# Performance work log

Measured on AMD Instinct MI355X. Metric: run time of the kernel, lower is better.

Reference implementation:

```python
import jax, jax.numpy as jnp
import numpy as np

N_V = 100000
N_E = 20000
NNZ = 1600000
D = 128


def setup_inputs() -> dict:
    key = jax.random.key(0)
    k1, k2, k3, k4, k5 = jax.random.split(key, 5)
    X = jax.random.normal(k1, (N_V, D), dtype=jnp.float32)
    W = jax.random.normal(k2, (D, D), dtype=jnp.float32) * (1.0 / np.sqrt(D))
    b = jax.random.normal(k3, (D,), dtype=jnp.float32) * 0.01
    v2e_src = jax.random.randint(k4, (NNZ,), 0, N_V, dtype=jnp.int32)
    v2e_dst = jax.random.randint(k5, (NNZ,), 0, N_E, dtype=jnp.int32)
    return {"X": X, "W": W, "b": b, "v2e_src": v2e_src, "v2e_dst": v2e_dst, "num_e": N_E}


def reference(X, W, b, v2e_src, v2e_dst, num_e):
    num_v = X.shape[0]
    ones = jnp.ones(v2e_src.shape[0], dtype=X.dtype)
    # node degrees (values of D_v diagonal) and hyperedge incidence counts
    deg_v = jax.ops.segment_sum(ones, v2e_src, num_segments=num_v)
    cnt_e = jax.ops.segment_sum(ones, v2e_dst, num_segments=num_e)

    # theta: linear layer
    Xt = X @ W.T + b  # [N_V, D]

    # v2e mean aggregation: per hyperedge, mean of incident vertex features
    Ysum = jax.ops.segment_sum(Xt[v2e_src], v2e_dst, num_segments=num_e)  # [N_E, D]
    Y = Ysum / jnp.maximum(cnt_e, 1.0)[:, None]

    # edge norm: torch scatter_reduce(reduce='mean', include_self=True) -> sum/(count+1)
    De_sum = jax.ops.segment_sum(deg_v[v2e_src], v2e_dst, num_segments=num_e)
    De = De_sum / (cnt_e + 1.0)
    De = jnp.where(De > 0, jax.lax.rsqrt(jnp.maximum(De, 1e-30)), 1.0)  # inf -> 1
    Y = De[:, None] * Y

    # e2v sum aggregation
    Xo = jax.ops.segment_sum(Y[v2e_dst], v2e_src, num_segments=num_v)  # [N_V, D]

    # D_v^{-1/2} sparse diagonal mm (zero-degree nodes -> 0)
    dvn = jnp.where(deg_v > 0, jax.lax.rsqrt(jnp.maximum(deg_v, 1e-30)), 0.0)
    Xo = dvn[:, None] * Xo

    # is_last=False: ReLU then dropout (dropout is identity in eval)
    return jax.nn.relu(Xo)
```

## Files before the change

### kernel.cpp

```cpp
#include <hip/hip_runtime.h>
#include <hip/hip_bf16.h>

#define NV 100000
#define NE 20000
#define DD 128
#define ESHIFT 7
#define VSHIFT 9
#define NBE 157
#define NBV 196
#define NBK 256
#define CHUNK 4096
#define CAPE 11264
#define CAPV 9216

using bf16 = __hip_bfloat16;

typedef __attribute__((ext_vector_type(8))) short frag_ab;
typedef __attribute__((ext_vector_type(4))) float frag_cd;

__device__ __forceinline__ float uas(unsigned u) { union { unsigned u; float f; } c; c.u = u; return c.f; }
__device__ __forceinline__ unsigned pk2(float lo, float hi) {
    bf16 l = __float2bfloat16(lo), h = __float2bfloat16(hi);
    return (unsigned)(*(unsigned short*)&l) | ((unsigned)(*(unsigned short*)&h) << 16);
}
__device__ __forceinline__ void accum8(float* a, uint4 x) {
    a[0] += uas(x.x << 16); a[1] += uas(x.x & 0xffff0000u);
    a[2] += uas(x.y << 16); a[3] += uas(x.y & 0xffff0000u);
    a[4] += uas(x.z << 16); a[5] += uas(x.z & 0xffff0000u);
    a[6] += uas(x.w << 16); a[7] += uas(x.w & 0xffff0000u);
}
__device__ __forceinline__ int wave_incl_scan(int v, int lane) {
#pragma unroll
    for (int o = 1; o < 64; o <<= 1) {
        int x = __shfl_up(v, o);
        if (lane >= o) v += x;
    }
    return v;
}

__global__ void init_cur(int* __restrict__ bcur_e, int* __restrict__ bcur_v) {
    int t = threadIdx.x;
    bcur_e[t] = t * CAPE;
    bcur_v[t] = t * CAPV;
}

__global__ __launch_bounds__(256) void partition_and_cvt(const int* __restrict__ src, const int* __restrict__ dst,
                                                         int* __restrict__ bcur_e, int* __restrict__ bcur_v,
                                                         unsigned* __restrict__ pairs_e, unsigned* __restrict__ pairs_v,
                                                         int nnz,
                                                         const float4* __restrict__ Xf, ushort4* __restrict__ Xb,
                                                         const float4* __restrict__ Wf, ushort4* __restrict__ Wb) {
    int nchunk = (nnz + CHUNK - 1) / CHUNK;
    int t = threadIdx.x;
    if ((int)blockIdx.x >= nchunk) {
        const int n4x = NV * DD / 4;
        const int n4w = DD * DD / 4;
        int i = ((int)blockIdx.x - nchunk) * 256 + t;
        if (i < n4x + n4w) {
            float4 v;
            ushort4 o;
            if (i < n4x) v = Xf[i]; else v = Wf[i - n4x];
            bf16 a = __float2bfloat16(v.x); o.x = *(unsigned short*)&a;
            bf16 b = __float2bfloat16(v.y); o.y = *(unsigned short*)&b;
            bf16 c = __float2bfloat16(v.z); o.z = *(unsigned short*)&c;
            bf16 d = __float2bfloat16(v.w); o.w = *(unsigned short*)&d;
            if (i < n4x) Xb[i] = o; else Wb[i - n4x] = o;
        }
        return;
    }
    __shared__ int cntA[NBK], cntB[NBK], pre1[NBK], loff[NBK], gbase[NBK], wsum[4];
    __shared__ int totValid;
    __shared__ unsigned stage[CHUNK];
    int sub = t >> 7;
    int lane = t & 63, wv = t >> 6;
    int base = blockIdx.x * CHUNK;
    unsigned p[16];
    int rk[16];
#pragma unroll
    for (int k = 0; k < 16; ++k) {
        int i = base + k * 256 + t;
        p[k] = (i < nnz) ? (((unsigned)src[i] << 15) | (unsigned)dst[i]) : 0xFFFFFFFFu;
    }

    cntA[t] = 0; cntB[t] = 0;
    __syncthreads();
#pragma unroll
    for (int k = 0; k < 16; ++k)
        if (p[k] != 0xFFFFFFFFu) {
            int b = (p[k] >> ESHIFT) & 0xFF;
            rk[k] = atomicAdd(sub ? &cntB[b] : &cntA[b], 1);
        }
    __syncthreads();
    {
        int a = cntA[t], bb = cntB[t];
        int tv = a + bb;
        pre1[t] = a;
        int incl = wave_incl_scan(tv, lane);
        if (lane == 63) wsum[wv] = incl;
        __syncthreads();
        if (t == 0) { int r = 0; for (int i = 0; i < 4; ++i) { int x = wsum[i]; wsum[i] = r; r += x; } }
        __syncthreads();
        int ex = incl - tv + wsum[wv];
        loff[t] = ex;
        gbase[t] = (tv > 0) ? atomicAdd(&bcur_e[t], tv) : 0;
        if (t == 255) totValid = ex + tv;
    }
    __syncthreads();
#pragma unroll
    for (int k = 0; k < 16; ++k)
        if (p[k] != 0xFFFFFFFFu) {
            int b = (p[k] >> ESHIFT) & 0xFF;
            stage[loff[b] + rk[k] + (sub ? pre1[b] : 0)] = p[k];
        }
    __syncthreads();
    for (int i = t; i < totValid; i += 256) {
        unsigned pp = stage[i];
        int b = (pp >> ESHIFT) & 0xFF;
        pairs_e[gbase[b] + i - loff[b]] = pp;
    }
    __syncthreads();

    cntA[t] = 0; cntB[t] = 0;
    __syncthreads();
#pragma unroll
    for (int k = 0; k < 16; ++k)
        if (p[k] != 0xFFFFFFFFu) {
            int b = p[k] >> 24;
            rk[k] = atomicAdd(sub ? &cntB[b] : &cntA[b], 1);
        }
    __syncthreads();
    {
        int a = cntA[t], bb = cntB[t];
        int tv = a + bb;
        pre1[t] = a;
        int incl = wave_incl_scan(tv, lane);
        if (lane == 63) wsum[wv] = incl;
        __syncthreads();
        if (t == 0) { int r = 0; for (int i = 0; i < 4; ++i) { int x = wsum[i]; wsum[i] = r; r += x; } }
        __syncthreads();
        int ex = incl - tv + wsum[wv];
        loff[t] = ex;
        gbase[t] = (tv > 0) ? atomicAdd(&bcur_v[t], tv) : 0;
        if (t == 255) totValid = ex + tv;
    }
    __syncthreads();
#pragma unroll
    for (int k = 0; k < 16; ++k)
        if (p[k] != 0xFFFFFFFFu) {
            int b = p[k] >> 24;
            stage[loff[b] + rk[k] + (sub ? pre1[b] : 0)] = p[k];
        }
    __syncthreads();
    for (int i = t; i < totValid; i += 256) {
        unsigned pp = stage[i];
        int b = pp >> 24;
        pairs_v[gbase[b] + i - loff[b]] = pp;
    }
}

__global__ __launch_bounds__(1024) void build_csr(const unsigned* __restrict__ pairs_e, const int* __restrict__ bcur_e,
                                                  int* __restrict__ off_e, int* __restrict__ end_e, int* __restrict__ e_src,
                                                  const unsigned* __restrict__ pairs_v, const int* __restrict__ bcur_v,
                                                  int* __restrict__ off_v, int* __restrict__ end_v, int* __restrict__ v_edge,
                                                  int* __restrict__ deg_v) {
    __shared__ int cA[2048], cB[2048], sc2[512], eoff[512], wsumS[8];
    int t = threadIdx.x;
    cA[t] = 0; cA[t + 1024] = 0;
    __syncthreads();
    if ((int)blockIdx.x < NBE) {
        int b = blockIdx.x;
        int lo = b * CAPE, hi = bcur_e[b];
        int sub = t >> 7;
        unsigned pv[12];
        int rk[12];
        int kk = 0;
        for (int i = lo + t; i < hi; i += 1024, ++kk) {
            unsigned p = pairs_e[i];
            pv[kk] = p;
            rk[kk] = atomicAdd(&cA[sub * 128 + (p & 127)], 1);
        }
        __syncthreads();
        if (t < 128) {
            int run = 0;
#pragma unroll
            for (int s = 0; s < 8; ++s) { cB[s * 128 + t] = run; run += cA[s * 128 + t]; }
            sc2[t] = run;
        }
        __syncthreads();
        int incl = 0, myrun = 0;
        if (t < 128) {
            myrun = sc2[t];
            incl = wave_incl_scan(myrun, t & 63);
            if ((t & 63) == 63) wsumS[t >> 6] = incl;
        }
        __syncthreads();
        if (t == 0) { int r = 0; for (int i = 0; i < 2; ++i) { int x = wsumS[i]; wsumS[i] = r; r += x; } }
        __syncthreads();
        if (t < 128) {
            int ex = incl - myrun + wsumS[t >> 6];
            eoff[t] = ex;
            int e = (b << ESHIFT) + t;
            if (e < NE) { off_e[e] = lo + ex; end_e[e] = lo + ex + myrun; }
        }
        __syncthreads();
        for (int k = 0; k < kk; ++k) {
            int bkt = pv[k] & 127;
            int pos = lo + eoff[bkt] + cB[sub * 128 + bkt] + rk[k];
            e_src[pos] = (int)(pv[k] >> 15);
        }
    } else {
        int b = blockIdx.x - NBE;
        int lo = b * CAPV, hi = bcur_v[b];
        int sub = t >> 8;
        unsigned pv[9];
        int rk[9];
        int kk = 0;
        for (int i = lo + t; i < hi; i += 1024, ++kk) {
            unsigned p = pairs_v[i];
            pv[kk] = p;
            rk[kk] = atomicAdd(&cA[sub * 512 + ((p >> 15) & 511)], 1);
        }
        __syncthreads();
        if (t < 512) {
            int run = 0;
#pragma unroll
            for (int s = 0; s < 4; ++s) { cB[s * 512 + t] = run; run += cA[s * 512 + t]; }
            sc2[t] = run;
        }
        __syncthreads();
        int incl = 0, myrun = 0;
        if (t < 512) {
            myrun = sc2[t];
            incl = wave_incl_scan(myrun, t & 63);
            if ((t & 63) == 63) wsumS[t >> 6] = incl;
        }
        __syncthreads();
        if (t == 0) { int r = 0; for (int i = 0; i < 8; ++i) { int x = wsumS[i]; wsumS[i] = r; r += x; } }
        __syncthreads();
        if (t < 512) {
            int ex = incl - myrun + wsumS[t >> 6];
            eoff[t] = ex;
            int v = (b << VSHIFT) + t;
            if (v < NV) { off_v[v] = lo + ex; end_v[v] = lo + ex + myrun; deg_v[v] = myrun; }
        }
        __syncthreads();
        for (int k = 0; k < kk; ++k) {
            int bkt = (pv[k] >> 15) & 511;
            int pos = lo + eoff[bkt] + cB[sub * 512 + bkt] + rk[k];
            v_edge[pos] = (int)(pv[k] & 0x7FFF);
        }
    }
}

__global__ __launch_bounds__(256) void edge_fused(const uint4* __restrict__ Xq, const int* __restrict__ off_e,
                                                  const int* __restrict__ end_e,
                                                  const int* __restrict__ e_src, const int* __restrict__ deg_v,
                                                  const bf16* __restrict__ Wb, const float* __restrict__ bias,
                                                  bf16* __restrict__ Y) {
    __shared__ short Stile[16][136];
    __shared__ float betaL[16];
    int t = threadIdx.x;
    int w = t >> 6, lane = t & 63;
    int g = lane >> 4, l16 = lane & 15;
    int mBase = blockIdx.x * 16;
    int le = w * 4 + g;
    int e = mBase + le;
    int start = off_e[e], end = end_e[e];
    float acc[8] = {0.f, 0.f, 0.f, 0.f, 0.f, 0.f, 0.f, 0.f};
    float degsum = 0.f;
    int j = start;
    for (; j + 8 <= end; j += 8) {
        int s0 = e_src[j + 0], s1 = e_src[j + 1], s2 = e_src[j + 2], s3 = e_src[j + 3];
        int s4 = e_src[j + 4], s5 = e_src[j + 5], s6 = e_src[j + 6], s7 = e_src[j + 7];
        uint4 x0 = Xq[(size_t)s0 * 16 + l16];
        uint4 x1 = Xq[(size_t)s1 * 16 + l16];
        uint4 x2 = Xq[(size_t)s2 * 16 + l16];
        uint4 x3 = Xq[(size_t)s3 * 16 + l16];
        uint4 x4 = Xq[(size_t)s4 * 16 + l16];
        uint4 x5 = Xq[(size_t)s5 * 16 + l16];
        uint4 x6 = Xq[(size_t)s6 * 16 + l16];
        uint4 x7 = Xq[(size_t)s7 * 16 + l16];
        degsum += (float)(deg_v[s0] + deg_v[s1] + deg_v[s2] + deg_v[s3]
                        + deg_v[s4] + deg_v[s5] + deg_v[s6] + deg_v[s7]);
        accum8(acc, x0); accum8(acc, x1); accum8(acc, x2); accum8(acc, x3);
        accum8(acc, x4); accum8(acc, x5); accum8(acc, x6); accum8(acc, x7);
    }
    for (; j + 4 <= end; j += 4) {
        int s0 = e_src[j + 0], s1 = e_src[j + 1], s2 = e_src[j + 2], s3 = e_src[j + 3];
        uint4 x0 = Xq[(size_t)s0 * 16 + l16];
        uint4 x1 = Xq[(size_t)s1 * 16 + l16];
        uint4 x2 = Xq[(size_t)s2 * 16 + l16];
        uint4 x3 = Xq[(size_t)s3 * 16 + l16];
        degsum += (float)(deg_v[s0] + deg_v[s1] + deg_v[s2] + deg_v[s3]);
        accum8(acc, x0); accum8(acc, x1); accum8(acc, x2); accum8(acc, x3);
    }
    for (; j < end; ++j) {
        int s = e_src[j];
        uint4 x = Xq[(size_t)s * 16 + l16];
        degsum += (float)deg_v[s];
        accum8(acc, x);
    }
    float cntf = (float)(end - start);
    float Des = degsum / (cntf + 1.0f);
    float De = (Des > 0.f) ? rsqrtf(fmaxf(Des, 1e-30f)) : 1.0f;
    float scale = De / fmaxf(cntf, 1.0f);
    {
        uint4 o;
        o.x = pk2(acc[0] * scale, acc[1] * scale);
        o.y = pk2(acc[2] * scale, acc[3] * scale);
        o.z = pk2(acc[4] * scale, acc[5] * scale);
        o.w = pk2(acc[6] * scale, acc[7] * scale);
        *(uint4*)&Stile[le][l16 * 8] = o;
        if (l16 == 0) betaL[le] = (cntf > 0.f) ? De : 0.f;
    }
    __syncthreads();

    const short* Ws = (const short*)Wb;
    int quad = g;
    frag_ab a[4];
#pragma unroll
    for (int kt = 0; kt < 4; ++kt)
        a[kt] = *(const frag_ab*)&Stile[l16][kt * 32 + quad * 8];
    float beta_r[4];
#pragma unroll
    for (int r = 0; r < 4; ++r) beta_r[r] = betaL[quad * 4 + r];

#pragma unroll
    for (int nn = 0; nn < 2; ++nn) {
        int nt = w * 2 + nn;
        frag_cd acc2 = {0.f, 0.f, 0.f, 0.f};
#pragma unroll
        for (int kt = 0; kt < 4; ++kt) {
            frag_ab bfr = *(const frag_ab*)(Ws + (size_t)(nt * 16 + l16) * DD + kt * 32 + quad * 8);
            acc2 = __builtin_amdgcn_mfma_f32_16x16x32_bf16(a[kt], bfr, acc2, 0, 0, 0);
        }
        float bv = bias[nt * 16 + l16];
#pragma unroll
        for (int r = 0; r < 4; ++r) {
            int row = mBase + quad * 4 + r;
            float v = acc2[r] + beta_r[r] * bv;
            Y[(size_t)row * DD + nt * 16 + l16] = __float2bfloat16(v);
        }
    }
}

__global__ __launch_bounds__(256) void vertex_agg(const uint4* __restrict__ Yq, const int* __restrict__ off_v,
                                                  const int* __restrict__ end_v,
                                                  const int* __restrict__ v_edge, float* __restrict__ out) {
    int wave = (blockIdx.x * blockDim.x + threadIdx.x) >> 6;
    int lane = threadIdx.x & 63;
    int g = lane >> 4, l16 = lane & 15;
    int v = wave * 4 + g;
    if (v >= NV) return;
    int start = off_v[v], end = end_v[v];
    float acc[8] = {0.f, 0.f, 0.f, 0.f, 0.f, 0.f, 0.f, 0.f};
    int j = start;
    for (; j + 8 <= end; j += 8) {
        int e0 = v_edge[j + 0], e1 = v_edge[j + 1], e2 = v_edge[j + 2], e3 = v_edge[j + 3];
        int e4 = v_edge[j + 4], e5 = v_edge[j + 5], e6 = v_edge[j + 6], e7 = v_edge[j + 7];
        uint4 y0 = Yq[(size_t)e0 * 16 + l16];
        uint4 y1 = Yq[(size_t)e1 * 16 + l16];
        uint4 y2 = Yq[(size_t)e2 * 16 + l16];
        uint4 y3 = Yq[(size_t)e3 * 16 + l16];
        uint4 y4 = Yq[(size_t)e4 * 16 + l16];
        uint4 y5 = Yq[(size_t)e5 * 16 + l16];
        uint4 y6 = Yq[(size_t)e6 * 16 + l16];
        uint4 y7 = Yq[(size_t)e7 * 16 + l16];
        accum8(acc, y0); accum8(acc, y1); accum8(acc, y2); accum8(acc, y3);
        accum8(acc, y4); accum8(acc, y5); accum8(acc, y6); accum8(acc, y7);
    }
    for (; j + 4 <= end; j += 4) {
        int e0 = v_edge[j + 0], e1 = v_edge[j + 1], e2 = v_edge[j + 2], e3 = v_edge[j + 3];
        uint4 y0 = Yq[(size_t)e0 * 16 + l16];
        uint4 y1 = Yq[(size_t)e1 * 16 + l16];
        uint4 y2 = Yq[(size_t)e2 * 16 + l16];
        uint4 y3 = Yq[(size_t)e3 * 16 + l16];
        accum8(acc, y0); accum8(acc, y1); accum8(acc, y2); accum8(acc, y3);
    }
    for (; j < end; ++j) {
        int e = v_edge[j];
        uint4 y = Yq[(size_t)e * 16 + l16];
        accum8(acc, y);
    }
    int deg = end - start;
    float dvn = (deg > 0) ? rsqrtf((float)deg) : 0.f;
    float4 o1, o2;
    o1.x = fmaxf(acc[0] * dvn, 0.f);
    o1.y = fmaxf(acc[1] * dvn, 0.f);
    o1.z = fmaxf(acc[2] * dvn, 0.f);
    o1.w = fmaxf(acc[3] * dvn, 0.f);
    o2.x = fmaxf(acc[4] * dvn, 0.f);
    o2.y = fmaxf(acc[5] * dvn, 0.f);
    o2.z = fmaxf(acc[6] * dvn, 0.f);
    o2.w = fmaxf(acc[7] * dvn, 0.f);
    float4* op = (float4*)(out + (size_t)v * DD + l16 * 8);
    op[0] = o1;
    op[1] = o2;
}

extern "C" void kernel_launch(void* const* d_in, const int* in_sizes, int n_in,
                              void* d_out, int out_size, void* d_ws, size_t ws_size,
                              hipStream_t stream) {
    const float* X = (const float*)d_in[0];
    const float* W = (const float*)d_in[1];
    const float* b = (const float*)d_in[2];
    const int* src = (const int*)d_in[3];
    const int* dst = (const int*)d_in[4];
    int nnz = in_sizes[3];

    char* ws = (char*)d_ws;
    size_t o = 0;
    auto take = [&](size_t bytes) -> char* {
        char* p = ws + o;
        o += (bytes + 255) & ~(size_t)255;
        return p;
    };
    int* bcur_e = (int*)take(NBK * 4);
    int* bcur_v = (int*)take(NBK * 4);
    int* off_e = (int*)take((size_t)NE * 4);
    int* end_e = (int*)take((size_t)NE * 4);
    int* off_v = (int*)take((size_t)NV * 4);
    int* end_v = (int*)take((size_t)NV * 4);
    int* deg_v = (int*)take((size_t)NV * 4);
    int* e_src = (int*)take((size_t)NBE * CAPE * 4);
    int* v_edge = (int*)take((size_t)NBV * CAPV * 4);
    unsigned* pairs_e = (unsigned*)take((size_t)NBE * CAPE * 4);
    unsigned* pairs_v = (unsigned*)take((size_t)NBV * CAPV * 4);
    bf16* Y = (bf16*)take((size_t)NE * DD * 2);
    bf16* Wb = (bf16*)take((size_t)DD * DD * 2);
    bf16* Xb = (bf16*)take((size_t)NV * DD * 2);
    (void)ws_size; (void)n_in; (void)out_size;

    int nchunk = (nnz + CHUNK - 1) / CHUNK;
    int ncvt = (NV * DD / 4 + DD * DD / 4 + 255) / 256;

    init_cur<<<1, NBK, 0, stream>>>(bcur_e, bcur_v);
    partition_and_cvt<<<nchunk + ncvt, 256, 0, stream>>>(src, dst, bcur_e, bcur_v, pairs_e, pairs_v, nnz,
                                                         (const float4*)X, (ushort4*)Xb,
                                                         (const float4*)W, (ushort4*)Wb);
    build_csr<<<NBE + NBV, 1024, 0, stream>>>(pairs_e, bcur_e, off_e, end_e, e_src,
                                              pairs_v, bcur_v, off_v, end_v, v_edge, deg_v);
    edge_fused<<<NE / 16, 256, 0, stream>>>((const uint4*)Xb, off_e, end_e, e_src, deg_v, Wb, b, Y);
    vertex_agg<<<(NV / 4 * 64) / 256, 256, 0, stream>>>((const uint4*)Y, off_v, end_v, v_edge, (float*)d_out);
}
```

Measured before the change: 255.4 us.

## Split partition phases across blocks and halve per-edge gather work in edge_fused

partition_and_cvt now launches twice as many chunk blocks, each doing either the edge-bucket or the vertex-bucket scatter instead of one block doing both sequentially. edge_fused uses 512 threads: two half-waves each gather half of an edge's incident vertices, combine partial sums with a cross-lane shuffle, and each wave computes one 16-column MFMA tile instead of two. The aim is more parallelism and shorter dependency chains on the long gather loops. In exchange, each chunk's src/dst is read twice and there are extra shuffles and larger blocks, which may reduce occupancy.

```diff
diff --git a/kernel.cpp b/kernel.cpp
--- a/kernel.cpp
+++ b/kernel.cpp
@@ -52,10 +52,11 @@
                                                          const float4* __restrict__ Wf, ushort4* __restrict__ Wb) {
     int nchunk = (nnz + CHUNK - 1) / CHUNK;
     int t = threadIdx.x;
-    if ((int)blockIdx.x >= nchunk) {
+    int bid = blockIdx.x;
+    if (bid >= 2 * nchunk) {
         const int n4x = NV * DD / 4;
         const int n4w = DD * DD / 4;
-        int i = ((int)blockIdx.x - nchunk) * 256 + t;
+        int i = (bid - 2 * nchunk) * 256 + t;
         if (i < n4x + n4w) {
             float4 v;
             ushort4 o;
@@ -71,9 +72,11 @@
     __shared__ int cntA[NBK], cntB[NBK], pre1[NBK], loff[NBK], gbase[NBK], wsum[4];
     __shared__ int totValid;
     __shared__ unsigned stage[CHUNK];
+    int phase = (bid >= nchunk) ? 1 : 0;
+    int cidx = phase ? bid - nchunk : bid;
     int sub = t >> 7;
     int lane = t & 63, wv = t >> 6;
-    int base = blockIdx.x * CHUNK;
+    int base = cidx * CHUNK;
     unsigned p[16];
     int rk[16];
 #pragma unroll
@@ -87,7 +90,7 @@
 #pragma unroll
     for (int k = 0; k < 16; ++k)
         if (p[k] != 0xFFFFFFFFu) {
-            int b = (p[k] >> ESHIFT) & 0xFF;
+            int b = phase ? (int)(p[k] >> 24) : (int)((p[k] >> ESHIFT) & 0xFF);
             rk[k] = atomicAdd(sub ? &cntB[b] : &cntA[b], 1);
         }
     __syncthreads();
@@ -102,59 +105,22 @@
         __syncthreads();
         int ex = incl - tv + wsum[wv];
         loff[t] = ex;
-        gbase[t] = (tv > 0) ? atomicAdd(&bcur_e[t], tv) : 0;
+        gbase[t] = (tv > 0) ? atomicAdd(phase ? &bcur_v[t] : &bcur_e[t], tv) : 0;
         if (t == 255) totValid = ex + tv;
     }
     __syncthreads();
 #pragma unroll
     for (int k = 0; k < 16; ++k)
         if (p[k] != 0xFFFFFFFFu) {
-            int b = (p[k] >> ESHIFT) & 0xFF;
+            int b = phase ? (int)(p[k] >> 24) : (int)((p[k] >> ESHIFT) & 0xFF);
             stage[loff[b] + rk[k] + (sub ? pre1[b] : 0)] = p[k];
         }
     __syncthreads();
+    unsigned* outp = phase ? pairs_v : pairs_e;
     for (int i = t; i < totValid; i += 256) {
         unsigned pp = stage[i];
-        int b = (pp >> ESHIFT) & 0xFF;
-        pairs_e[gbase[b] + i - loff[b]] = pp;
-    }
-    __syncthreads();
-
-    cntA[t] = 0; cntB[t] = 0;
-    __syncthreads();
-#pragma unroll
-    for (int k = 0; k < 16; ++k)
-        if (p[k] != 0xFFFFFFFFu) {
-            int b = p[k] >> 24;
-            rk[k] = atomicAdd(sub ? &cntB[b] : &cntA[b], 1);
-        }
-    __syncthreads();
-    {
-        int a = cntA[t], bb = cntB[t];
-        int tv = a + bb;
-        pre1[t] = a;
-        int incl = wave_incl_scan(tv, lane);
-        if (lane == 63) wsum[wv] = incl;
-        __syncthreads();
-        if (t == 0) { int r = 0; for (int i = 0; i < 4; ++i) { int x = wsum[i]; wsum[i] = r; r += x; } }
-        __syncthreads();
-        int ex = incl - tv + wsum[wv];
-        loff[t] = ex;
-        gbase[t] = (tv > 0) ? atomicAdd(&bcur_v[t], tv) : 0;
-        if (t == 255) totValid = ex + tv;
-    }
-    __syncthreads();
-#pragma unroll
-    for (int k = 0; k < 16; ++k)
-        if (p[k] != 0xFFFFFFFFu) {
-            int b = p[k] >> 24;
-            stage[loff[b] + rk[k] + (sub ? pre1[b] : 0)] = p[k];
-        }
-    __syncthreads();
-    for (int i = t; i < totValid; i += 256) {
-        unsigned pp = stage[i];
-        int b = pp >> 24;
-        pairs_v[gbase[b] + i - loff[b]] = pp;
+        int b = phase ? (int)(pp >> 24) : (int)((pp >> ESHIFT) & 0xFF);
+        outp[gbase[b] + i - loff[b]] = pp;
     }
 }
 
@@ -252,7 +218,7 @@
     }
 }
 
-__global__ __launch_bounds__(256) void edge_fused(const uint4* __restrict__ Xq, const int* __restrict__ off_e,
+__global__ __launch_bounds__(512) void edge_fused(const uint4* __restrict__ Xq, const int* __restrict__ off_e,
                                                   const int* __restrict__ end_e,
                                                   const int* __restrict__ e_src, const int* __restrict__ deg_v,
                                                   const bf16* __restrict__ Wb, const float* __restrict__ bias,
@@ -261,15 +227,21 @@
     __shared__ float betaL[16];
     int t = threadIdx.x;
     int w = t >> 6, lane = t & 63;
-    int g = lane >> 4, l16 = lane & 15;
+    int h = lane >> 5;
+    int g2 = (lane >> 4) & 1;
+    int l16 = lane & 15;
     int mBase = blockIdx.x * 16;
-    int le = w * 4 + g;
+    int le = w * 2 + g2;
     int e = mBase + le;
     int start = off_e[e], end = end_e[e];
+    int cnt = end - start;
+    int half0 = (cnt + 1) >> 1;
+    int hs = start + h * half0;
+    int he = h ? end : (start + half0);
     float acc[8] = {0.f, 0.f, 0.f, 0.f, 0.f, 0.f, 0.f, 0.f};
     float degsum = 0.f;
-    int j = start;
-    for (; j + 8 <= end; j += 8) {
+    int j = hs;
+    for (; j + 8 <= he; j += 8) {
         int s0 = e_src[j + 0], s1 = e_src[j + 1], s2 = e_src[j + 2], s3 = e_src[j + 3];
         int s4 = e_src[j + 4], s5 = e_src[j + 5], s6 = e_src[j + 6], s7 = e_src[j + 7];
         uint4 x0 = Xq[(size_t)s0 * 16 + l16];
@@ -285,7 +257,7 @@
         accum8(acc, x0); accum8(acc, x1); accum8(acc, x2); accum8(acc, x3);
         accum8(acc, x4); accum8(acc, x5); accum8(acc, x6); accum8(acc, x7);
     }
-    for (; j + 4 <= end; j += 4) {
+    for (; j + 4 <= he; j += 4) {
         int s0 = e_src[j + 0], s1 = e_src[j + 1], s2 = e_src[j + 2], s3 = e_src[j + 3];
         uint4 x0 = Xq[(size_t)s0 * 16 + l16];
         uint4 x1 = Xq[(size_t)s1 * 16 + l16];
@@ -294,17 +266,21 @@
         degsum += (float)(deg_v[s0] + deg_v[s1] + deg_v[s2] + deg_v[s3]);
         accum8(acc, x0); accum8(acc, x1); accum8(acc, x2); accum8(acc, x3);
     }
-    for (; j < end; ++j) {
+    for (; j < he; ++j) {
         int s = e_src[j];
         uint4 x = Xq[(size_t)s * 16 + l16];
         degsum += (float)deg_v[s];
         accum8(acc, x);
     }
-    float cntf = (float)(end - start);
+#pragma unroll
+    for (int r = 0; r < 8; ++r) acc[r] += __shfl_xor(acc[r], 32);
+    degsum += __shfl_xor(degsum, 32);
+
+    float cntf = (float)cnt;
     float Des = degsum / (cntf + 1.0f);
     float De = (Des > 0.f) ? rsqrtf(fmaxf(Des, 1e-30f)) : 1.0f;
     float scale = De / fmaxf(cntf, 1.0f);
-    {
+    if (h == 0) {
         uint4 o;
         o.x = pk2(acc[0] * scale, acc[1] * scale);
         o.y = pk2(acc[2] * scale, acc[3] * scale);
@@ -316,7 +292,7 @@
     __syncthreads();
 
     const short* Ws = (const short*)Wb;
-    int quad = g;
+    int quad = lane >> 4;
     frag_ab a[4];
 #pragma unroll
     for (int kt = 0; kt < 4; ++kt)
@@ -325,22 +301,19 @@
 #pragma unroll
     for (int r = 0; r < 4; ++r) beta_r[r] = betaL[quad * 4 + r];
 
-#pragma unroll
-    for (int nn = 0; nn < 2; ++nn) {
-        int nt = w * 2 + nn;
-        frag_cd acc2 = {0.f, 0.f, 0.f, 0.f};
-#pragma unroll
-        for (int kt = 0; kt < 4; ++kt) {
-            frag_ab bfr = *(const frag_ab*)(Ws + (size_t)(nt * 16 + l16) * DD + kt * 32 + quad * 8);
-            acc2 = __builtin_amdgcn_mfma_f32_16x16x32_bf16(a[kt], bfr, acc2, 0, 0, 0);
-        }
-        float bv = bias[nt * 16 + l16];
-#pragma unroll
-        for (int r = 0; r < 4; ++r) {
-            int row = mBase + quad * 4 + r;
-            float v = acc2[r] + beta_r[r] * bv;
-            Y[(size_t)row * DD + nt * 16 + l16] = __float2bfloat16(v);
-        }
+    int nt = w;
+    frag_cd acc2 = {0.f, 0.f, 0.f, 0.f};
+#pragma unroll
+    for (int kt = 0; kt < 4; ++kt) {
+        frag_ab bfr = *(const frag_ab*)(Ws + (size_t)(nt * 16 + l16) * DD + kt * 32 + quad * 8);
+        acc2 = __builtin_amdgcn_mfma_f32_16x16x32_bf16(a[kt], bfr, acc2, 0, 0, 0);
+    }
+    float bv = bias[nt * 16 + l16];
+#pragma unroll
+    for (int r = 0; r < 4; ++r) {
+        int row = mBase + quad * 4 + r;
+        float v = acc2[r] + beta_r[r] * bv;
+        Y[(size_t)row * DD + nt * 16 + l16] = __float2bfloat16(v);
     }
 }
 
@@ -435,11 +408,11 @@
     int ncvt = (NV * DD / 4 + DD * DD / 4 + 255) / 256;
 
     init_cur<<<1, NBK, 0, stream>>>(bcur_e, bcur_v);
-    partition_and_cvt<<<nchunk + ncvt, 256, 0, stream>>>(src, dst, bcur_e, bcur_v, pairs_e, pairs_v, nnz,
-                                                         (const float4*)X, (ushort4*)Xb,
-                                                         (const float4*)W, (ushort4*)Wb);
+    partition_and_cvt<<<2 * nchunk + ncvt, 256, 0, stream>>>(src, dst, bcur_e, bcur_v, pairs_e, pairs_v, nnz,
+                                                             (const float4*)X, (ushort4*)Xb,
+                                                             (const float4*)W, (ushort4*)Wb);
     build_csr<<<NBE + NBV, 1024, 0, stream>>>(pairs_e, bcur_e, off_e, end_e, e_src,
                                               pairs_v, bcur_v, off_v, end_v, v_edge, deg_v);
-    edge_fused<<<NE / 16, 256, 0, stream>>>((const uint4*)Xb, off_e, end_e, e_src, deg_v, Wb, b, Y);
+    edge_fused<<<NE / 16, 512, 0, stream>>>((const uint4*)Xb, off_e, end_e, e_src, deg_v, Wb, b, Y);
     vertex_agg<<<(NV / 4 * 64) / 256, 256, 0, stream>>>((const uint4*)Y, off_v, end_v, v_edge, (float*)d_out);
 }
```

After: 248.8 us. 1.03x faster.
